# Kernel optimization log

Measured on AMD Instinct MI355X. Metric: run time of the kernel, lower is better.

Reference implementation:

```python
import jax, jax.numpy as jnp
import numpy as np

N = 524288
MAXV = 8  # rect-rect intersection has at most 8 vertices
EPS = 1e-8


def setup_inputs() -> dict:
    key = jax.random.key(0)
    k1, k2, k3 = jax.random.split(key, 3)
    return {
        "box": jax.random.normal(k1, (N, 11), jnp.float32),
        "box_target": jax.random.normal(k2, (N, 11), jnp.float32),
        "weight": jax.random.uniform(k3, (N, 11), jnp.float32),
        "avg_factor": N // 2,
    }


def decode_box(box):
    # [x,y,z,logW,logL,logH,sin,cos,v...] -> [x,y,z,W,L,H,yaw,v...]
    yaw = jnp.arctan2(box[..., 6], box[..., 7])
    return jnp.concatenate(
        [box[..., :3], jnp.exp(box[..., 3:6]), yaw[..., None], box[..., 8:]], axis=-1)


def get_rect_vertices(bev):
    # bev: (5,) = [cx, cy, w, l, yaw] -> (4, 2) corners, CCW, rotated about center
    cx, cy, w, l, yaw = bev[0], bev[1], bev[2], bev[3], bev[4]
    dx, dy = w / 2, l / 2
    lx = jnp.stack([-dx, dx, dx, -dx])
    ly = jnp.stack([-dy, -dy, dy, dy])
    s, c = jnp.sin(yaw), jnp.cos(yaw)
    return jnp.stack([lx * c - ly * s + cx, lx * s + ly * c + cy], axis=-1)


def clip_halfplane(poly, count, a, b):
    # Sutherland-Hodgman clip of poly (MAXV,2) with `count` valid verts
    # against left side of directed edge a->b. Fixed-size buffer + mask.
    d = b - a  # (2,)
    idx = jnp.arange(MAXV)
    cnt = jnp.maximum(count, 1)
    prev = poly[(idx - 1) % cnt]
    cur = poly

    def is_left(p):
        return d[0] * (p[..., 1] - a[1]) - d[1] * (p[..., 0] - a[0]) >= 0

    cur_in, prev_in = is_left(cur), is_left(prev)
    num = (a[0] - prev[:, 0]) * d[1] - (a[1] - prev[:, 1]) * d[0]
    den = (cur[:, 0] - prev[:, 0]) * d[1] - (cur[:, 1] - prev[:, 1]) * d[0] + EPS
    ip = prev + (num / den)[:, None] * (cur - prev)  # edge/halfplane intersection
    valid = idx < count
    emit_ip = valid & (prev_in ^ cur_in)   # crossing edge -> emit intersection
    emit_cur = valid & cur_in              # inside vertex -> emit it
    # interleave per-input-edge outputs in original order (ip, then cur)
    pts = jnp.stack([ip, cur], axis=1).reshape(2 * MAXV, 2)
    emit = jnp.stack([emit_ip, emit_cur], axis=1).reshape(2 * MAXV)
    pos = jnp.where(emit, jnp.cumsum(emit) - 1, MAXV)  # compact valid pts to front
    out = jnp.zeros((MAXV, 2), poly.dtype).at[pos].set(
        jnp.where(emit[:, None], pts, 0.0), mode="drop")
    return out, jnp.minimum(emit.sum(), MAXV).astype(jnp.int32)


def poly_area(poly, count):
    # shoelace over the `count` valid vertices
    idx = jnp.arange(MAXV)
    nxt = poly[(idx + 1) % jnp.maximum(count, 1)]
    cross = jnp.where(idx < count, poly[:, 0] * nxt[:, 1] - poly[:, 1] * nxt[:, 0], 0.0)
    return jnp.abs(cross.sum() / 2.0)


def giou_one(bev1, bev2):
    v1 = get_rect_vertices(bev1)  # (4,2)
    v2 = get_rect_vertices(bev2)
    poly = jnp.zeros((MAXV, 2), bev1.dtype).at[:4].set(v1)
    count = jnp.int32(4)
    for i in range(4):  # clip subject rect by 4 half-planes of clip rect
        poly, count = clip_halfplane(poly, count, v2[i], v2[(i + 1) % 4])
        count = jnp.where(count < 3, 0, count)  # degenerate -> empty (original break)
    inter = poly_area(poly, count)
    area1 = bev1[2] * bev1[3]
    area2 = bev2[2] * bev2[3]
    union = area1 + area2 - inter
    allp = jnp.concatenate([v1, v2], axis=0)
    enclosing = (allp[:, 0].max() - allp[:, 0].min()) * (allp[:, 1].max() - allp[:, 1].min())
    iou = inter / (union + EPS)
    return iou - (enclosing - union) / (enclosing + EPS)


def _bev(dec):
    return jnp.stack([dec[:, 0], dec[:, 1], dec[:, 3], dec[:, 4], dec[:, 6]], axis=-1)


def reference(box, box_target, weight, avg_factor):
    af = max(float(avg_factor), 1.0)
    # L1 box loss (reg_weights are all 1.0 per init defaults)
    loss_box = (jnp.abs(box - box_target) * weight).sum() / af
    # rotated BEV GIoU loss
    bev_p = _bev(decode_box(box))
    bev_t = _bev(decode_box(box_target))
    giou = jax.vmap(giou_one)(bev_p, bev_t)
    loss_giou = (1.0 - giou).sum() / af
    return loss_box, loss_giou
```

## Files before the change

kernel.cpp:

```cpp
#include <hip/hip_runtime.h>

#define BLOCK 128
#define ITERS 4
#define EPSF 1e-8f

typedef float f4u __attribute__((ext_vector_type(4), aligned(4)));

struct Row9 { f4u b0, b1, b2, t0, t1, t2, w0, w1, w2; };

__device__ __forceinline__ Row9 load_row(const float* __restrict__ box,
                                         const float* __restrict__ tgt,
                                         const float* __restrict__ wgt,
                                         int row) {
    const size_t r = (size_t)row * 11;
    Row9 R;
    R.b0 = *(const f4u*)(box + r); R.b1 = *(const f4u*)(box + r + 4); R.b2 = *(const f4u*)(box + r + 7);
    R.t0 = *(const f4u*)(tgt + r); R.t1 = *(const f4u*)(tgt + r + 4); R.t2 = *(const f4u*)(tgt + r + 7);
    R.w0 = *(const f4u*)(wgt + r); R.w1 = *(const f4u*)(wgt + r + 4); R.w2 = *(const f4u*)(wgt + r + 7);
    return R;
}

__device__ __forceinline__ float safe_rcp(float d) {
    float sd = (fabsf(d) > 1e-30f) ? d : copysignf(1e-30f, d);
    return __frcp_rn(sd);
}

__device__ __forceinline__ float clip_len(float px, float py,
                                          float rdx, float rdy,
                                          float hx, float hy) {
    float t1x = (-hx - px) * rdx, t2x = (hx - px) * rdx;
    float t1y = (-hy - py) * rdy, t2y = (hy - py) * rdy;
    float tmin = fmaxf(fmaxf(fminf(t1x, t2x), fminf(t1y, t2y)), 0.f);
    float tmax = fminf(fminf(fmaxf(t1x, t2x), fmaxf(t1y, t2y)), 1.f);
    return fmaxf(tmax - tmin, 0.f);
}

__device__ __forceinline__ void box_compute(const Row9& R, float& l1out, float& gout)
{
    f4u b0 = R.b0, b1 = R.b1, b2 = R.b2;
    f4u t0 = R.t0, t1 = R.t1, t2 = R.t2;
    f4u w0 = R.w0, w1 = R.w1, w2 = R.w2;

    float lb = 0.f;
    lb += fabsf(b0.x - t0.x) * w0.x;
    lb += fabsf(b0.y - t0.y) * w0.y;
    lb += fabsf(b0.z - t0.z) * w0.z;
    lb += fabsf(b0.w - t0.w) * w0.w;
    lb += fabsf(b1.x - t1.x) * w1.x;
    lb += fabsf(b1.y - t1.y) * w1.y;
    lb += fabsf(b1.z - t1.z) * w1.z;
    lb += fabsf(b1.w - t1.w) * w1.w;
    lb += fabsf(b2.y - t2.y) * w2.y;
    lb += fabsf(b2.z - t2.z) * w2.z;
    lb += fabsf(b2.w - t2.w) * w2.w;
    l1out = lb;

    float cx1 = b0.x, cy1 = b0.y, cx2 = t0.x, cy2 = t0.y;
    float w1v = __expf(b0.w), l1v = __expf(b1.x);
    float w2v = __expf(t0.w), l2v = __expf(t1.x);
    float r1 = rsqrtf(fmaxf(b1.z * b1.z + b1.w * b1.w, 1e-30f));
    float s1 = b1.z * r1, c1 = b1.w * r1;
    float r2 = rsqrtf(fmaxf(t1.z * t1.z + t1.w * t1.w, 1e-30f));
    float s2 = t1.z * r2, c2 = t1.w * r2;

    float hx1 = 0.5f * w1v, hy1 = 0.5f * l1v;
    float hx2 = 0.5f * w2v, hy2 = 0.5f * l2v;

    float e1x = fabsf(hx1 * c1) + fabsf(hy1 * s1);
    float e1y = fabsf(hx1 * s1) + fabsf(hy1 * c1);
    float e2x = fabsf(hx2 * c2) + fabsf(hy2 * s2);
    float e2y = fabsf(hx2 * s2) + fabsf(hy2 * c2);
    float enc = (fmaxf(cx1 + e1x, cx2 + e2x) - fminf(cx1 - e1x, cx2 - e2x))
              * (fmaxf(cy1 + e1y, cy2 + e2y) - fminf(cy1 - e1y, cy2 - e2y));

    float dxw = cx1 - cx2, dyw = cy1 - cy2;
    float txl =  c2 * dxw + s2 * dyw;
    float tyl = -s2 * dxw + c2 * dyw;
    float cr_ = c1 * c2 + s1 * s2;
    float sr_ = s1 * c2 - c1 * s2;

    float ax_ = hx1 * cr_, ay_ = hx1 * sr_;
    float bx_ = hy1 * sr_, by_ = hy1 * cr_;
    float q0x = txl - ax_ + bx_, q0y = tyl - ay_ - by_;
    float q1x = txl + ax_ + bx_, q1y = tyl + ay_ - by_;
    float q2x = txl + ax_ - bx_, q2y = tyl + ay_ + by_;
    float q3x = txl - ax_ - bx_, q3y = tyl - ay_ + by_;

    float inter2 = 0.f;
    {
        float d01x = 2.f * ax_, d01y = 2.f * ay_;
        float d12x = -2.f * bx_, d12y = 2.f * by_;
        float r01x = safe_rcp(d01x), r01y = safe_rcp(d01y);
        float r12x = safe_rcp(d12x), r12y = safe_rcp(d12y);
        float L0 = clip_len(q0x, q0y,  r01x,  r01y, hx2, hy2);
        inter2 += L0 * (q0x * d01y - q0y * d01x);
        float L1 = clip_len(q1x, q1y,  r12x,  r12y, hx2, hy2);
        inter2 += L1 * (q1x * d12y - q1y * d12x);
        float L2 = clip_len(q2x, q2y, -r01x, -r01y, hx2, hy2);
        inter2 += L2 * (q2y * d01x - q2x * d01y);
        float L3 = clip_len(q3x, q3y, -r12x, -r12y, hx2, hy2);
        inter2 += L3 * (q3y * d12x - q3x * d12y);
    }
    {
        float zx = -hx2 - txl, zy = -hy2 - tyl;
        float u0x =  cr_ * zx + sr_ * zy;
        float u0y = -sr_ * zx + cr_ * zy;
        float E0x =  2.f * hx2 * cr_, E0y = -2.f * hx2 * sr_;
        float E1x =  2.f * hy2 * sr_, E1y =  2.f * hy2 * cr_;
        float u1x = u0x + E0x, u1y = u0y + E0y;
        float u2x = u1x + E1x, u2y = u1y + E1y;
        float u3x = u0x + E1x, u3y = u0y + E1y;
        float re0x = safe_rcp(E0x), re0y = safe_rcp(E0y);
        float re1x = safe_rcp(E1x), re1y = safe_rcp(E1y);
        float tsum = 0.f;
        tsum += clip_len(u0x, u0y,  re0x,  re0y, hx1, hy1);
        tsum += clip_len(u1x, u1y,  re1x,  re1y, hx1, hy1);
        tsum += clip_len(u2x, u2y, -re0x, -re0y, hx1, hy1);
        tsum += clip_len(u3x, u3y, -re1x, -re1y, hx1, hy1);
        inter2 += 2.f * hx2 * hy2 * tsum;
    }

    float inter = 0.5f * fabsf(inter2);
    float areaU = w1v * l1v + w2v * l2v - inter;
    float iou = __fdividef(inter, areaU + EPSF);
    float giou = iou - __fdividef(enc - areaU, enc + EPSF);
    gout = 1.f - giou;
}

__global__ __launch_bounds__(BLOCK) void box_loss_main(
    const float* __restrict__ box, const float* __restrict__ tgt,
    const float* __restrict__ wgt, int n, int T, float* __restrict__ partials)
{
    __shared__ float red[4];

    const int tid = threadIdx.x;
    const int i0 = blockIdx.x * BLOCK + tid;
    const int i1 = i0 + T, i2 = i1 + T, i3 = i2 + T;
    const bool v0 = i0 < n, v1 = i1 < n, v2 = i2 < n, v3 = i3 < n;

    Row9 A = load_row(box, tgt, wgt, v0 ? i0 : 0);
    Row9 B = load_row(box, tgt, wgt, v1 ? i1 : 0);

    float sumL1 = 0.f, sumG = 0.f;
    float l1, g;

    Row9 C = load_row(box, tgt, wgt, v2 ? i2 : 0);
    box_compute(A, l1, g);
    sumL1 += v0 ? l1 : 0.f;  sumG += v0 ? g : 0.f;

    A = load_row(box, tgt, wgt, v3 ? i3 : 0);
    box_compute(B, l1, g);
    sumL1 += v1 ? l1 : 0.f;  sumG += v1 ? g : 0.f;

    box_compute(C, l1, g);
    sumL1 += v2 ? l1 : 0.f;  sumG += v2 ? g : 0.f;

    box_compute(A, l1, g);
    sumL1 += v3 ? l1 : 0.f;  sumG += v3 ? g : 0.f;

#pragma unroll
    for (int off = 32; off > 0; off >>= 1) {
        sumL1 += __shfl_down(sumL1, off);
        sumG  += __shfl_down(sumG, off);
    }
    const int wave = tid >> 6, lane = tid & 63;
    if (lane == 0) { red[wave] = sumL1; red[2 + wave] = sumG; }
    __syncthreads();
    if (tid == 0) {
        partials[2 * (size_t)blockIdx.x]     = red[0] + red[1];
        partials[2 * (size_t)blockIdx.x + 1] = red[2] + red[3];
    }
}

__global__ __launch_bounds__(256) void box_loss_final(
    const float* __restrict__ partials, int nblk,
    const int* __restrict__ avg_factor, float* __restrict__ out)
{
    __shared__ float red[8];
    float a = 0.f, g = 0.f;
    for (int i = threadIdx.x; i < nblk; i += 256) {
        a += partials[2 * (size_t)i];
        g += partials[2 * (size_t)i + 1];
    }
#pragma unroll
    for (int off = 32; off > 0; off >>= 1) {
        a += __shfl_down(a, off);
        g += __shfl_down(g, off);
    }
    const int wave = threadIdx.x >> 6, lane = threadIdx.x & 63;
    if (lane == 0) { red[wave] = a; red[4 + wave] = g; }
    __syncthreads();
    if (threadIdx.x == 0) {
        float af = (float)(*avg_factor);
        if (af < 1.f) af = 1.f;
        out[0] = (red[0] + red[1] + red[2] + red[3]) / af;
        out[1] = (red[4] + red[5] + red[6] + red[7]) / af;
    }
}

extern "C" void kernel_launch(void* const* d_in, const int* in_sizes, int n_in,
                              void* d_out, int out_size, void* d_ws, size_t ws_size,
                              hipStream_t stream) {
    const float* box = (const float*)d_in[0];
    const float* tgt = (const float*)d_in[1];
    const float* wgt = (const float*)d_in[2];
    const int*   af  = (const int*)d_in[3];
    float* out = (float*)d_out;
    float* partials = (float*)d_ws;

    int n = in_sizes[0] / 11;
    int nblk = (n + BLOCK * ITERS - 1) / (BLOCK * ITERS);
    if (nblk < 1) nblk = 1;
    int T = nblk * BLOCK;

    hipLaunchKernelGGL(box_loss_main, dim3(nblk), dim3(BLOCK), 0, stream,
                       box, tgt, wgt, n, T, partials);
    hipLaunchKernelGGL(box_loss_final, dim3(1), dim3(256), 0, stream,
                       partials, nblk, af, out);
}
```

Before: 20.11 us.

## Fuse final reduction into main kernel via atomics and retune block shape

Drops the separate single-block final reduction kernel. Each block now scales its partial sums by the average factor and atomically adds them into the output, which is zeroed by a memset beforehand. Block size goes to 256 threads with 2 rows per thread and a launch-bounds occupancy hint, giving 1024 blocks and 1024 atomics per output. This removes one kernel launch and the serial tail, but adds a memset, atomic contention and a nondeterministic float summation order.

```diff
diff --git a/kernel.cpp b/kernel.cpp
--- a/kernel.cpp
+++ b/kernel.cpp
@@ -1,7 +1,7 @@
 #include <hip/hip_runtime.h>
 
-#define BLOCK 128
-#define ITERS 4
+#define BLOCK 256
+#define ITERS 2
 #define EPSF 1e-8f
 
 typedef float f4u __attribute__((ext_vector_type(4), aligned(4)));
@@ -127,36 +127,28 @@
     gout = 1.f - giou;
 }
 
-__global__ __launch_bounds__(BLOCK) void box_loss_main(
+__global__ __launch_bounds__(BLOCK, 4) void box_loss_main(
     const float* __restrict__ box, const float* __restrict__ tgt,
-    const float* __restrict__ wgt, int n, int T, float* __restrict__ partials)
+    const float* __restrict__ wgt, int n, int T,
+    const int* __restrict__ avg_factor, float* __restrict__ out)
 {
-    __shared__ float red[4];
+    __shared__ float red[8];
 
     const int tid = threadIdx.x;
-    const int i0 = blockIdx.x * BLOCK + tid;
-    const int i1 = i0 + T, i2 = i1 + T, i3 = i2 + T;
-    const bool v0 = i0 < n, v1 = i1 < n, v2 = i2 < n, v3 = i3 < n;
-
-    Row9 A = load_row(box, tgt, wgt, v0 ? i0 : 0);
-    Row9 B = load_row(box, tgt, wgt, v1 ? i1 : 0);
+    const int iA = blockIdx.x * BLOCK + tid;
+    const int iB = iA + T;
+    const bool hasA = iA < n, hasB = iB < n;
 
     float sumL1 = 0.f, sumG = 0.f;
     float l1, g;
 
-    Row9 C = load_row(box, tgt, wgt, v2 ? i2 : 0);
-    box_compute(A, l1, g);
-    sumL1 += v0 ? l1 : 0.f;  sumG += v0 ? g : 0.f;
-
-    A = load_row(box, tgt, wgt, v3 ? i3 : 0);
-    box_compute(B, l1, g);
-    sumL1 += v1 ? l1 : 0.f;  sumG += v1 ? g : 0.f;
-
-    box_compute(C, l1, g);
-    sumL1 += v2 ? l1 : 0.f;  sumG += v2 ? g : 0.f;
+    Row9 A = load_row(box, tgt, wgt, hasA ? iA : 0);
+    Row9 B = load_row(box, tgt, wgt, hasB ? iB : 0);
 
     box_compute(A, l1, g);
-    sumL1 += v3 ? l1 : 0.f;  sumG += v3 ? g : 0.f;
+    sumL1 += hasA ? l1 : 0.f;  sumG += hasA ? g : 0.f;
+    box_compute(B, l1, g);
+    sumL1 += hasB ? l1 : 0.f;  sumG += hasB ? g : 0.f;
 
 #pragma unroll
     for (int off = 32; off > 0; off >>= 1) {
@@ -164,37 +156,17 @@
         sumG  += __shfl_down(sumG, off);
     }
     const int wave = tid >> 6, lane = tid & 63;
-    if (lane == 0) { red[wave] = sumL1; red[2 + wave] = sumG; }
+    if (lane == 0) { red[wave] = sumL1; red[4 + wave] = sumG; }
     __syncthreads();
     if (tid == 0) {
-        partials[2 * (size_t)blockIdx.x]     = red[0] + red[1];
-        partials[2 * (size_t)blockIdx.x + 1] = red[2] + red[3];
-    }
-}
-
-__global__ __launch_bounds__(256) void box_loss_final(
-    const float* __restrict__ partials, int nblk,
-    const int* __restrict__ avg_factor, float* __restrict__ out)
-{
-    __shared__ float red[8];
-    float a = 0.f, g = 0.f;
-    for (int i = threadIdx.x; i < nblk; i += 256) {
-        a += partials[2 * (size_t)i];
-        g += partials[2 * (size_t)i + 1];
-    }
-#pragma unroll
-    for (int off = 32; off > 0; off >>= 1) {
-        a += __shfl_down(a, off);
-        g += __shfl_down(g, off);
-    }
-    const int wave = threadIdx.x >> 6, lane = threadIdx.x & 63;
-    if (lane == 0) { red[wave] = a; red[4 + wave] = g; }
-    __syncthreads();
-    if (threadIdx.x == 0) {
         float af = (float)(*avg_factor);
         if (af < 1.f) af = 1.f;
-        out[0] = (red[0] + red[1] + red[2] + red[3]) / af;
-        out[1] = (red[4] + red[5] + red[6] + red[7]) / af;
+        float inv = __frcp_rn(af);
+        float a = (red[0] + red[1] + red[2] + red[3]) * (1.f / af);
+        float gg = (red[4] + red[5] + red[6] + red[7]) * (1.f / af);
+        (void)inv;
+        atomicAdd(&out[0], a);
+        atomicAdd(&out[1], gg);
     }
 }
 
@@ -206,15 +178,13 @@
     const float* wgt = (const float*)d_in[2];
     const int*   af  = (const int*)d_in[3];
     float* out = (float*)d_out;
-    float* partials = (float*)d_ws;
 
     int n = in_sizes[0] / 11;
     int nblk = (n + BLOCK * ITERS - 1) / (BLOCK * ITERS);
     if (nblk < 1) nblk = 1;
     int T = nblk * BLOCK;
 
+    hipMemsetAsync(out, 0, 2 * sizeof(float), stream);
     hipLaunchKernelGGL(box_loss_main, dim3(nblk), dim3(BLOCK), 0, stream,
-                       box, tgt, wgt, n, T, partials);
-    hipLaunchKernelGGL(box_loss_final, dim3(1), dim3(256), 0, stream,
-                       partials, nblk, af, out);
+                       box, tgt, wgt, n, T, af, out);
 }
```

Measured after the change: 44.13 us. +119.5%, slower.
